# Performance work log

Hardware: AMD Instinct MI355X
Metric: run time of the kernel (lower is better)

Reference implementation:

```python
import jax, jax.numpy as jnp
import numpy as np

B = 64        # batch
N = 1024      # num_nodes
D_IN = 2      # input feature dim per node
U = 64        # num_units (hidden)
K = 2         # max_diffusion_step


def setup_inputs() -> dict:
    key = jax.random.key(0)
    ks = jax.random.split(key, 8)
    inputs = jax.random.normal(ks[0], (B, N * D_IN), dtype=jnp.float32)
    hx = jax.random.normal(ks[1], (B, N * U), dtype=jnp.float32)
    # random-walk style supports: nonnegative, row-normalized -> stable Chebyshev recursion
    a0 = jax.random.uniform(ks[2], (N, N), dtype=jnp.float32)
    a1 = jax.random.uniform(ks[3], (N, N), dtype=jnp.float32)
    support0 = a0 / jnp.sum(a0, axis=1, keepdims=True)
    support1 = a1 / jnp.sum(a1, axis=1, keepdims=True)
    num_matrices = 2 * K + 1            # len(supports)*K + 1 = 5
    in_sz = (D_IN + U) * num_matrices   # 330
    # xavier-normal init
    std_o = float(np.sqrt(2.0 / (in_sz + 2 * U)))
    std_u = float(np.sqrt(2.0 / (in_sz + U)))
    weights_output = jax.random.normal(ks[4], (in_sz, 2 * U), dtype=jnp.float32) * std_o
    weights_update = jax.random.normal(ks[5], (in_sz, U), dtype=jnp.float32) * std_u
    biases_output = jnp.ones((2 * U,), dtype=jnp.float32)
    biases_update = jnp.zeros((U,), dtype=jnp.float32)
    return {"inputs": inputs, "hx": hx, "support0": support0, "support1": support1,
            "weights_output": weights_output, "biases_output": biases_output,
            "weights_update": weights_update, "biases_update": biases_update}


def _gconv(x_cat, supports, W, b, out_size):
    # x_cat: [B, N, F]  -> Chebyshev diffusion series then dense projection
    Bsz, Nn, F = x_cat.shape
    x0 = x_cat.transpose(1, 2, 0).reshape(Nn, F * Bsz)  # [N, F*B]
    xs = [x0]
    for S in supports:
        x1 = S @ x0
        xs.append(x1)
        xk1, xk2 = x1, x0
        for _ in range(2, K + 1):
            x2 = 2.0 * (S @ xk1) - xk2
            xs.append(x2)
            xk1, xk2 = x2, xk1
    M = len(xs)                                         # num_matrices
    x = jnp.stack(xs, axis=0)                           # [M, N, F*B]
    x = x.reshape(M, Nn, F, Bsz).transpose(3, 1, 2, 0)  # [B, N, F, M]
    x = x.reshape(Bsz * Nn, F * M)
    y = x @ W + b                                       # [B*N, out_size]
    return y.reshape(Bsz, Nn * out_size)


def reference(inputs, hx, support0, support1, weights_output, biases_output,
              weights_update, biases_update):
    supports = (support0, support1)
    xi = inputs.reshape(B, N, D_IN)
    hs = hx.reshape(B, N, U)
    cat = jnp.concatenate([xi, hs], axis=2)             # [B, N, D_IN+U]
    value = jax.nn.sigmoid(_gconv(cat, supports, weights_output, biases_output, 2 * U))
    value = value.reshape(B, N, 2 * U)
    r = value[..., :U].reshape(B, N * U)
    u = value[..., U:].reshape(B, N * U)
    cat2 = jnp.concatenate([xi, (r * hx).reshape(B, N, U)], axis=2)
    c = jnp.tanh(_gconv(cat2, supports, weights_update, biases_update, U))
    return u * hx + (1.0 - u) * c
```

## Files before the change

kernel.cpp:

```cpp
#include <hip/hip_runtime.h>


typedef unsigned short u16;
typedef unsigned int u32;
typedef short s16x8 __attribute__((ext_vector_type(8)));
typedef float f32x4 __attribute__((ext_vector_type(4)));
typedef u16 u16x4 __attribute__((ext_vector_type(4)));

#define NN 1024
#define NB 64
#define NF 66
#define NCOLS 4224
#define KPAD 352
#define ASTRIDE 360

__device__ __forceinline__ u16 f2bf(float f) {
  u32 u = __builtin_bit_cast(u32, f);
  u = (u + 0x7fffu + ((u >> 16) & 1u)) >> 16;
  return (u16)u;
}
__device__ __forceinline__ float bf2f(u16 h) {
  u32 u = ((u32)h) << 16;
  return __builtin_bit_cast(float, u);
}

__device__ __forceinline__ void gload16(const void* g, void* l) {
  __builtin_amdgcn_global_load_lds(
      (const __attribute__((address_space(1))) u32*)g,
      (__attribute__((address_space(3))) u32*)l, 16, 0, 0);
}

#define CHEB_WAIT(N)                                      \
  do {                                                    \
    asm volatile("s_waitcnt vmcnt(" #N ")" ::: "memory"); \
    __builtin_amdgcn_s_barrier();                         \
    asm volatile("" ::: "memory");                        \
  } while (0)


__global__ __launch_bounds__(256) void pack_supports(
    const float* __restrict__ s0, const float* __restrict__ s1,
    u16* __restrict__ d0, u16* __restrict__ d1,
    u16* __restrict__ t0, u16* __restrict__ t1) {
  __shared__ float tile[64][65];
  const int z = blockIdx.y;
  const float* S = z ? s1 : s0;
  u16* D = z ? d1 : d0;
  u16* T = z ? t1 : t0;
  const int r0 = (blockIdx.x >> 4) * 64, c0 = (blockIdx.x & 15) * 64;
  const int t = threadIdx.x;
  int cc4 = (t & 15) * 4, rr = t >> 4;
#pragma unroll
  for (int p = 0; p < 4; p++) {
    int r = p * 16 + rr;
    f32x4 v = *(const f32x4*)(S + (size_t)(r0 + r) * NN + c0 + cc4);
    tile[r][cc4] = v.x; tile[r][cc4 + 1] = v.y;
    tile[r][cc4 + 2] = v.z; tile[r][cc4 + 3] = v.w;
    u16x4 o;
    o.x = f2bf(v.x); o.y = f2bf(v.y); o.z = f2bf(v.z); o.w = f2bf(v.w);
    *(u16x4*)&D[(size_t)(r0 + r) * NN + c0 + cc4] = o;
  }
  __syncthreads();
  int rr4 = (t & 15) * 4, cc = t >> 4;
#pragma unroll
  for (int p = 0; p < 4; p++) {
    int c = p * 16 + cc;
    u16x4 o;
    o.x = f2bf(tile[rr4][c]);     o.y = f2bf(tile[rr4 + 1][c]);
    o.z = f2bf(tile[rr4 + 2][c]); o.w = f2bf(tile[rr4 + 3][c]);
    *(u16x4*)&T[(size_t)(c0 + c) * NN + r0 + rr4] = o;
  }
}

__global__ __launch_bounds__(64) void pack_wf(
    const float* __restrict__ Wo, const float* __restrict__ Wu,
    u16* __restrict__ WF1, u16* __restrict__ WF2) {
  const int c = blockIdx.x;
  int j = blockIdx.y;
  const float* W; u16* WF; int ldo, nj;
  if (j < 8) { W = Wo; WF = WF1; ldo = 128; nj = 8; }
  else       { j -= 8; W = Wu; WF = WF2; ldo = 64; nj = 4; }
  const int lane = threadIdx.x;
  const int o = j * 16 + (lane & 15);
  const int kpb = c * 32 + (lane >> 4) * 8;
  u16 vals[8];
#pragma unroll
  for (int e = 0; e < 8; e++) {
    const int kp = kpb + e;
    float v = 0.f;
    if (kp < 330) {
      const int m = kp / 66;
      const int f = kp - m * 66;
      const float* Wrow = W + (size_t)(f * 5) * ldo + o;
      if (m == 0)      v = Wrow[0] - Wrow[2 * ldo] - Wrow[4 * ldo];
      else if (m == 2) v = 2.f * Wrow[2 * ldo];
      else if (m == 4) v = 2.f * Wrow[4 * ldo];
      else             v = Wrow[(size_t)m * ldo];
    }
    vals[e] = f2bf(v);
  }
  u16* dst = WF + (((size_t)(c * nj + j) << 6) + lane) * 8;
#pragma unroll
  for (int e = 0; e < 8; e++) dst[e] = vals[e];
}

__global__ __launch_bounds__(256) void pack_x0(
    const float* __restrict__ inp, const float* __restrict__ hx,
    u16* __restrict__ x0t, u16* __restrict__ x0pt) {
  __shared__ float tile[64][65];
  int n0 = blockIdx.x * 64, b = blockIdx.y, t = threadIdx.x;
  if (t < 32) {
    const int f = t >> 4;
    const int n4 = (t & 15) * 4;
    const float* src = inp + b * 2048 + (n0 + n4) * 2 + f;
    u16x4 o;
    o.x = f2bf(src[0]); o.y = f2bf(src[2]); o.z = f2bf(src[4]); o.w = f2bf(src[6]);
    size_t off = (size_t)(f * 64 + b) * NN + n0 + n4;
    *(u16x4*)(x0t + off) = o;
    *(u16x4*)(x0pt + off) = o;
  }
  int u4 = (t & 15) * 4, r0 = t >> 4;
#pragma unroll
  for (int p = 0; p < 4; p++) {
    int row = p * 16 + r0;
    f32x4 v = *(const f32x4*)(hx + ((size_t)b << 16) + (size_t)(n0 + row) * 64 + u4);
    tile[row][u4] = v.x; tile[row][u4 + 1] = v.y;
    tile[row][u4 + 2] = v.z; tile[row][u4 + 3] = v.w;
  }
  __syncthreads();
  int n4 = (t & 15) * 4, uu0 = t >> 4;
#pragma unroll
  for (int p = 0; p < 4; p++) {
    int u = p * 16 + uu0;
    u16x4 o;
    o.x = f2bf(tile[n4][u]);     o.y = f2bf(tile[n4 + 1][u]);
    o.z = f2bf(tile[n4 + 2][u]); o.w = f2bf(tile[n4 + 3][u]);
    *(u16x4*)&x0t[(size_t)((2 + u) * 64 + b) * NN + n0 + n4] = o;
  }
}


__device__ __forceinline__ void gemm128_core(
    const u16* __restrict__ A, const u16* __restrict__ Xi, u16* __restrict__ Xo,
    int m0, int n0, int t, u16* AsB, u16* BsB) {
  const int lane = t & 63;
  const int w = t >> 6;

  const int swz = ((lane & 3) ^ ((lane >> 3) & 3)) * 8;
  const int rl = lane >> 2;
  const u16* pA0 = A + (size_t)(m0 + w * 32 + rl) * NN + swz;
  const u16* pA1 = pA0 + (size_t)16 * NN;
  const u16* pB0 = Xi + (size_t)(n0 + w * 32 + rl) * NN + swz;
  const u16* pB1 = pB0 + (size_t)16 * NN;
  const int db0 = (w * 32) * 32;
  const int db1 = (w * 32 + 16) * 32;

  const int wm = (w >> 1) * 64;
  const int wn = (w & 1) * 64;
  const int fr = lane & 15;
  const int q = lane >> 4;
  const int fo = (q ^ ((fr >> 1) & 3)) * 8;

  f32x4 acc[4][4];
#pragma unroll
  for (int i = 0; i < 4; i++)
#pragma unroll
    for (int j = 0; j < 4; j++) acc[i][j] = f32x4{0.f, 0.f, 0.f, 0.f};

  auto stage = [&](u16* dA, u16* dB) {
    gload16(pA0, dA + db0);
    gload16(pA1, dA + db1);
    gload16(pB0, dB + db0);
    gload16(pB1, dB + db1);
    pA0 += 32; pA1 += 32; pB0 += 32; pB1 += 32;
  };
  auto compute = [&](const u16* cA, const u16* cB) {
    s16x8 af[4], bfr[4];
#pragma unroll
    for (int i = 0; i < 4; i++)
      af[i] = *(const s16x8*)&cA[(wm + i * 16 + fr) * 32 + fo];
#pragma unroll
    for (int j = 0; j < 4; j++)
      bfr[j] = *(const s16x8*)&cB[(wn + j * 16 + fr) * 32 + fo];
#pragma unroll
    for (int i = 0; i < 4; i++)
#pragma unroll
      for (int j = 0; j < 4; j++)
        acc[i][j] = __builtin_amdgcn_mfma_f32_16x16x32_bf16(af[i], bfr[j], acc[i][j], 0, 0, 0);
  };

  u16* a0 = AsB;  u16* a1 = AsB + 128 * 32;  u16* a2 = AsB + 2 * 128 * 32;
  u16* b0 = BsB;  u16* b1 = BsB + 128 * 32;  u16* b2 = BsB + 2 * 128 * 32;

  stage(a0, b0);
  stage(a1, b1);
#pragma unroll 1
  for (int it = 0; it < 10; it++) {
    CHEB_WAIT(4); stage(a2, b2); compute(a0, b0);
    CHEB_WAIT(4); stage(a0, b0); compute(a1, b1);
    CHEB_WAIT(4); stage(a1, b1); compute(a2, b2);
  }
  CHEB_WAIT(4); compute(a0, b0);
  CHEB_WAIT(0); compute(a1, b1);

  const int nr0 = (lane >> 4) << 2;
#pragma unroll
  for (int i = 0; i < 4; i++) {
    const int node = m0 + wm + i * 16 + nr0;
#pragma unroll
    for (int j = 0; j < 4; j++) {
      const int colg = n0 + wn + j * 16 + fr;
      f32x4 c = acc[i][j];
      u16x4 o;
      o.x = f2bf(c.x); o.y = f2bf(c.y); o.z = f2bf(c.z); o.w = f2bf(c.w);
      *(u16x4*)&Xo[(size_t)colg * NN + node] = o;
    }
  }
}

__global__ __launch_bounds__(256) void sq_gemm(
    const u16* __restrict__ S0, const u16* __restrict__ S1,
    const u16* __restrict__ ST0, const u16* __restrict__ ST1,
    u16* __restrict__ SS0, u16* __restrict__ SS1) {
  __shared__ u16 As[2][128 * 64];
  __shared__ u16 Bs[2][128 * 64];
  const int t = threadIdx.x;
  const int lane = t & 63;
  const int w = t >> 6;
  const int lid = blockIdx.x;
  const int work = (lid & 7) * 16 + (lid >> 3);
  const int z = work >> 6;
  const int rr = work & 63;
  const int y = rr >> 3, x = rr & 7;
  const u16* A = z ? ST1 : ST0;
  const u16* Xi = z ? S1 : S0;
  u16* Xo = z ? SS1 : SS0;
  const int m0 = y * 128, n0 = x * 128;

  const int swz = ((lane & 7) ^ (lane >> 3)) * 8;
  const int rl = lane >> 3;
  const int rA = m0 + w * 32 + rl;
  const int rB = n0 + w * 32 + rl;
  const int dW = (w * 32) * 64;

  const int wm = (w >> 1) * 64;
  const int wn = (w & 1) * 64;
  const int fr = lane & 15;
  const int q = lane >> 4;

  f32x4 acc[4][4];
#pragma unroll
  for (int i = 0; i < 4; i++)
#pragma unroll
    for (int j = 0; j < 4; j++) acc[i][j] = f32x4{0.f, 0.f, 0.f, 0.f};

  auto stage = [&](int buf, int k0) {
    u16* a = &As[buf][0] + dW;
    u16* b = &Bs[buf][0] + dW;
#pragma unroll
    for (int g = 0; g < 4; g++) {
      gload16(A + (size_t)(rA + g * 8) * NN + k0 + swz, a + g * 8 * 64);
      gload16(Xi + (size_t)(rB + g * 8) * NN + k0 + swz, b + g * 8 * 64);
    }
  };
  auto compute = [&](int buf) {
    const u16* a = &As[buf][0];
    const u16* b = &Bs[buf][0];
#pragma unroll
    for (int kk = 0; kk < 2; kk++) {
      const int fo = ((kk * 4 + q) ^ (fr & 7)) * 8;
      s16x8 af[4], bfr[4];
#pragma unroll
      for (int i = 0; i < 4; i++)
        af[i] = *(const s16x8*)&a[(wm + i * 16 + fr) * 64 + fo];
#pragma unroll
      for (int j = 0; j < 4; j++)
        bfr[j] = *(const s16x8*)&b[(wn + j * 16 + fr) * 64 + fo];
#pragma unroll
      for (int i = 0; i < 4; i++)
#pragma unroll
        for (int j = 0; j < 4; j++)
          acc[i][j] = __builtin_amdgcn_mfma_f32_16x16x32_bf16(af[i], bfr[j], acc[i][j], 0, 0, 0);
    }
  };

  stage(0, 0);
  stage(1, 64);
#pragma unroll 1
  for (int tI = 0; tI < 14; tI++) {
    CHEB_WAIT(8);
    compute(tI & 1);
    __builtin_amdgcn_s_barrier();
    stage(tI & 1, (tI + 2) * 64);
  }
  CHEB_WAIT(8); compute(0);
  CHEB_WAIT(0); compute(1);

  const int nr0 = (lane >> 4) << 2;
#pragma unroll
  for (int i = 0; i < 4; i++) {
    const int node = m0 + wm + i * 16 + nr0;
#pragma unroll
    for (int j = 0; j < 4; j++) {
      const int colg = n0 + wn + j * 16 + fr;
      f32x4 c = acc[i][j];
      u16x4 o;
      o.x = f2bf(c.x); o.y = f2bf(c.y); o.z = f2bf(c.z); o.w = f2bf(c.w);
      *(u16x4*)&Xo[(size_t)colg * NN + node] = o;
    }
  }
}

__global__ __launch_bounds__(256, 3) void gconv_gemm(
    const u16* __restrict__ S0, const u16* __restrict__ S1,
    const u16* __restrict__ SS0, const u16* __restrict__ SS1,
    const u16* __restrict__ Xi,
    u16* __restrict__ X1, u16* __restrict__ X2,
    u16* __restrict__ X3, u16* __restrict__ X4) {
  __shared__ u16 As[3][128 * 32];
  __shared__ u16 Bs[3][128 * 32];
  const int lid = blockIdx.x;
  const int h = lid >= 528;
  const int l2 = h ? lid - 528 : lid;
  const int work = (l2 & 7) * 66 + (l2 >> 3);
  const int y = work & 7;
  const int tt = work >> 3;
  const int x = tt % 33;
  const int z = tt / 33;
  const u16* A = h ? (z ? SS1 : SS0) : (z ? S1 : S0);
  u16* Xo = h ? (z ? X4 : X2) : (z ? X3 : X1);
  gemm128_core(A, Xi, Xo, y * 128, x * 128, threadIdx.x, &As[0][0], &Bs[0][0]);
}


__device__ __forceinline__ void proj_stage(
    u16* A, const u16* __restrict__ X0, const u16* __restrict__ X1,
    const u16* __restrict__ X2, const u16* __restrict__ X3,
    const u16* __restrict__ X4, int b, int n0, int t) {
  u16x4 v[6][4];
#pragma unroll
  for (int i = 0; i < 6; i++) {
    const int idx = t + i * 256;
    if (idx < 1408) {
      const int kp0 = (idx >> 4) * 4;
      const int n4 = (idx & 15) * 4;
#pragma unroll
      for (int r = 0; r < 4; r++) {
        const int kp = kp0 + r;
        if (kp < 330) {
          const int m = kp / 66;
          const int f = kp - m * 66;
          const u16* Xm = m == 0 ? X0 : m == 1 ? X1 : m == 2 ? X2 : m == 3 ? X3 : X4;
          v[i][r] = *(const u16x4*)(Xm + (size_t)(f * 64 + b) * NN + n0 + n4);
        } else {
          v[i][r] = u16x4{0, 0, 0, 0};
        }
      }
    }
  }
#pragma unroll
  for (int i = 0; i < 6; i++) {
    const int idx = t + i * 256;
    if (idx < 1408) {
      const int kp0 = (idx >> 4) * 4;
      const int n4 = (idx & 15) * 4;
#pragma unroll
      for (int c = 0; c < 4; c++) {
        u16x4 o;
        o.x = v[i][0][c]; o.y = v[i][1][c]; o.z = v[i][2][c]; o.w = v[i][3][c];
        *(u16x4*)&A[(n4 + c) * ASTRIDE + kp0] = o;
      }
    }
  }
}

__global__ __launch_bounds__(256) void proj1(
    const u16* __restrict__ X0, const u16* __restrict__ X1, const u16* __restrict__ X2,
    const u16* __restrict__ X3, const u16* __restrict__ X4,
    const u16* __restrict__ WF, const float* __restrict__ bias,
    const float* __restrict__ hx, u16* __restrict__ X0p, float* __restrict__ uout) {
  __shared__ u16 A[64 * ASTRIDE];
  const int t = threadIdx.x;
  const int n0 = blockIdx.x * 64;
  const int b = blockIdx.y;
  proj_stage(A, X0, X1, X2, X3, X4, b, n0, t);
  __syncthreads();

  const int lane = t & 63;
  const int w = t >> 6;
  const int fr = lane & 15;
  const int q8 = (lane >> 4) * 8;
  const int nb = (w >> 1) * 32;
  const int jh = w & 1;
  const u16* arow = &A[(nb + fr) * ASTRIDE + q8];
  const u16* wfl = WF + (size_t)lane * 8;

  f32x4 acc[2][4];
#pragma unroll
  for (int ii = 0; ii < 2; ii++)
#pragma unroll
    for (int j = 0; j < 4; j++) acc[ii][j] = f32x4{0.f, 0.f, 0.f, 0.f};

  for (int c = 0; c < 11; c++) {
    s16x8 af[2];
#pragma unroll
    for (int ii = 0; ii < 2; ii++)
      af[ii] = *(const s16x8*)(arow + ii * 16 * ASTRIDE + c * 32);
#pragma unroll
    for (int j = 0; j < 4; j++) {
      const s16x8 bf = *(const s16x8*)(wfl + ((c * 8 + jh * 4 + j) << 9));
#pragma unroll
      for (int ii = 0; ii < 2; ii++)
        acc[ii][j] = __builtin_amdgcn_mfma_f32_16x16x32_bf16(af[ii], bf, acc[ii][j], 0, 0, 0);
    }
  }

  const int nl0 = (lane >> 4) * 4;
#pragma unroll
  for (int ii = 0; ii < 2; ii++) {
    const int n = n0 + nb + ii * 16 + nl0;
#pragma unroll
    for (int j = 0; j < 4; j++) {
      const int ol = j * 16 + fr;
      const float bs = bias[jh * 64 + ol];
      f32x4 v;
      v.x = 1.f / (1.f + __expf(-(acc[ii][j].x + bs)));
      v.y = 1.f / (1.f + __expf(-(acc[ii][j].y + bs)));
      v.z = 1.f / (1.f + __expf(-(acc[ii][j].z + bs)));
      v.w = 1.f / (1.f + __expf(-(acc[ii][j].w + bs)));
      if (jh == 0) {
        const float* hxp = hx + ((size_t)b << 16) + (size_t)n * 64 + ol;
        u16x4 s;
        s.x = f2bf(v.x * hxp[0 * 64]);
        s.y = f2bf(v.y * hxp[1 * 64]);
        s.z = f2bf(v.z * hxp[2 * 64]);
        s.w = f2bf(v.w * hxp[3 * 64]);
        *(u16x4*)&X0p[(size_t)((2 + ol) * 64 + b) * NN + n] = s;
      } else {
        float* up = uout + (((size_t)b << 10) + n) * 64 + ol;
        up[0 * 64] = v.x; up[1 * 64] = v.y; up[2 * 64] = v.z; up[3 * 64] = v.w;
      }
    }
  }
}

__global__ __launch_bounds__(256) void proj2(
    const u16* __restrict__ X0, const u16* __restrict__ X1, const u16* __restrict__ X2,
    const u16* __restrict__ X3, const u16* __restrict__ X4,
    const u16* __restrict__ WF, const float* __restrict__ bias,
    const float* __restrict__ hx, const float* uin, float* out) {
  __shared__ u16 A[64 * ASTRIDE];
  const int t = threadIdx.x;
  const int n0 = blockIdx.x * 64;
  const int b = blockIdx.y;
  proj_stage(A, X0, X1, X2, X3, X4, b, n0, t);
  __syncthreads();

  const int lane = t & 63;
  const int w = t >> 6;
  const int fr = lane & 15;
  const int q8 = (lane >> 4) * 8;
  const int nb = (w >> 1) * 32;
  const int jh = w & 1;
  const u16* arow = &A[(nb + fr) * ASTRIDE + q8];
  const u16* wfl = WF + (size_t)lane * 8;

  f32x4 acc[2][2];
#pragma unroll
  for (int ii = 0; ii < 2; ii++)
#pragma unroll
    for (int j = 0; j < 2; j++) acc[ii][j] = f32x4{0.f, 0.f, 0.f, 0.f};

  for (int c = 0; c < 11; c++) {
    s16x8 af[2];
#pragma unroll
    for (int ii = 0; ii < 2; ii++)
      af[ii] = *(const s16x8*)(arow + ii * 16 * ASTRIDE + c * 32);
#pragma unroll
    for (int j = 0; j < 2; j++) {
      const s16x8 bf = *(const s16x8*)(wfl + ((c * 4 + jh * 2 + j) << 9));
#pragma unroll
      for (int ii = 0; ii < 2; ii++)
        acc[ii][j] = __builtin_amdgcn_mfma_f32_16x16x32_bf16(af[ii], bf, acc[ii][j], 0, 0, 0);
    }
  }

  const int nl0 = (lane >> 4) * 4;
#pragma unroll
  for (int ii = 0; ii < 2; ii++) {
    const int n = n0 + nb + ii * 16 + nl0;
#pragma unroll
    for (int j = 0; j < 2; j++) {
      const int o = jh * 32 + j * 16 + fr;
      const float bs = bias[o];
      const size_t base = (((size_t)b << 10) + n) * 64 + o;
      float c0 = tanhf(acc[ii][j].x + bs);
      float c1 = tanhf(acc[ii][j].y + bs);
      float c2 = tanhf(acc[ii][j].z + bs);
      float c3 = tanhf(acc[ii][j].w + bs);
      float u0 = uin[base + 0 * 64], u1 = uin[base + 1 * 64];
      float u2 = uin[base + 2 * 64], u3 = uin[base + 3 * 64];
      float h0 = hx[base + 0 * 64], h1 = hx[base + 1 * 64];
      float h2 = hx[base + 2 * 64], h3 = hx[base + 3 * 64];
      out[base + 0 * 64] = u0 * h0 + (1.f - u0) * c0;
      out[base + 1 * 64] = u1 * h1 + (1.f - u1) * c1;
      out[base + 2 * 64] = u2 * h2 + (1.f - u2) * c2;
      out[base + 3 * 64] = u3 * h3 + (1.f - u3) * c3;
    }
  }
}


extern "C" void kernel_launch(void* const* d_in, const int* in_sizes, int n_in,
                              void* d_out, int out_size, void* d_ws, size_t ws_size,
                              hipStream_t stream) {
  (void)in_sizes; (void)n_in; (void)out_size; (void)ws_size;
  const float* inp = (const float*)d_in[0];
  const float* hx  = (const float*)d_in[1];
  const float* s0  = (const float*)d_in[2];
  const float* s1  = (const float*)d_in[3];
  const float* Wo  = (const float*)d_in[4];
  const float* bo  = (const float*)d_in[5];
  const float* Wu  = (const float*)d_in[6];
  const float* bu  = (const float*)d_in[7];
  float* out = (float*)d_out;

  char* p = (char*)d_ws;
  u16* Sb0 = (u16*)p; p += (size_t)NN * NN * 2;
  u16* Sb1 = (u16*)p; p += (size_t)NN * NN * 2;
  u16* SSb0 = (u16*)p; p += (size_t)NN * NN * 2;
  u16* SSb1 = (u16*)p; p += (size_t)NN * NN * 2;
  const size_t xbytes = (size_t)NCOLS * NN * 2;
  u16* X0T = (u16*)p; p += xbytes;
  u16* X1T = (u16*)p; p += xbytes;
  u16* X2T = (u16*)p; p += xbytes;
  u16* X3T = (u16*)p; p += xbytes;
  u16* X4T = (u16*)p; p += xbytes;
  u16* X0P = (u16*)p; p += xbytes;
  u16* WF1 = (u16*)p; p += (size_t)11 * 8 * 512 * 2;
  u16* WF2 = (u16*)p; p += (size_t)11 * 4 * 512 * 2;
  u16* ST0 = X1T;
  u16* ST1 = X3T;

  pack_supports<<<dim3(256, 2), dim3(256), 0, stream>>>(s0, s1, Sb0, Sb1, ST0, ST1);
  sq_gemm<<<dim3(128), dim3(256), 0, stream>>>(Sb0, Sb1, ST0, ST1, SSb0, SSb1);
  pack_wf<<<dim3(11, 12), dim3(64), 0, stream>>>(Wo, Wu, WF1, WF2);
  pack_x0<<<dim3(16, 64), dim3(256), 0, stream>>>(inp, hx, X0T, X0P);
  gconv_gemm<<<dim3(1056), dim3(256), 0, stream>>>(Sb0, Sb1, SSb0, SSb1, X0T,
                                                   X1T, X2T, X3T, X4T);
  proj1<<<dim3(16, 64), dim3(256), 0, stream>>>(X0T, X1T, X2T, X3T, X4T, WF1, bo, hx, X0P, out);
  gconv_gemm<<<dim3(1056), dim3(256), 0, stream>>>(Sb0, Sb1, SSb0, SSb1, X0P,
                                                   X1T, X2T, X3T, X4T);
  proj2<<<dim3(16, 64), dim3(256), 0, stream>>>(X0P, X1T, X2T, X3T, X4T, WF2, bu, hx, out, out);
}
```

Measured before the change: 267.0 us.

## Merge pack kernels into one launch and split proj staging into two phases

The three preprocessing kernels (support packing, weight packing, x0 packing) become one kernel that picks its role from the block index, removing two launches. The proj1/proj2 kernels now stage the 352-wide K dimension in two halves through a smaller shared buffer (stride 200 instead of 360). That cuts LDS use and, together with a launch-bounds hint of 6 blocks per CU, is meant to raise occupancy. The cost is an extra pair of barriers and a second staging pass in each projection block.

```diff
diff --git a/kernel.cpp b/kernel.cpp
--- a/kernel.cpp
+++ b/kernel.cpp
@@ -12,7 +12,7 @@
 #define NF 66
 #define NCOLS 4224
 #define KPAD 352
-#define ASTRIDE 360
+#define PSTRIDE 200
 
 __device__ __forceinline__ u16 f2bf(float f) {
   u32 u = __builtin_bit_cast(u32, f);
@@ -37,184 +37,107 @@
     asm volatile("" ::: "memory");                        \
   } while (0)
 
-
-__global__ __launch_bounds__(256) void pack_supports(
+__global__ __launch_bounds__(256) void pack_all(
     const float* __restrict__ s0, const float* __restrict__ s1,
-    u16* __restrict__ d0, u16* __restrict__ d1,
-    u16* __restrict__ t0, u16* __restrict__ t1) {
+    const float* __restrict__ inp, const float* __restrict__ hx,
+    const float* __restrict__ Wo, const float* __restrict__ Wu,
+    u16* __restrict__ Sb0, u16* __restrict__ Sb1,
+    u16* __restrict__ ST0, u16* __restrict__ ST1,
+    u16* __restrict__ x0t, u16* __restrict__ x0pt,
+    u16* __restrict__ WF1, u16* __restrict__ WF2) {
   __shared__ float tile[64][65];
-  const int z = blockIdx.y;
-  const float* S = z ? s1 : s0;
-  u16* D = z ? d1 : d0;
-  u16* T = z ? t1 : t0;
-  const int r0 = (blockIdx.x >> 4) * 64, c0 = (blockIdx.x & 15) * 64;
+  const int bid = blockIdx.x;
   const int t = threadIdx.x;
-  int cc4 = (t & 15) * 4, rr = t >> 4;
-#pragma unroll
-  for (int p = 0; p < 4; p++) {
-    int r = p * 16 + rr;
-    f32x4 v = *(const f32x4*)(S + (size_t)(r0 + r) * NN + c0 + cc4);
-    tile[r][cc4] = v.x; tile[r][cc4 + 1] = v.y;
-    tile[r][cc4 + 2] = v.z; tile[r][cc4 + 3] = v.w;
-    u16x4 o;
-    o.x = f2bf(v.x); o.y = f2bf(v.y); o.z = f2bf(v.z); o.w = f2bf(v.w);
-    *(u16x4*)&D[(size_t)(r0 + r) * NN + c0 + cc4] = o;
-  }
-  __syncthreads();
-  int rr4 = (t & 15) * 4, cc = t >> 4;
-#pragma unroll
-  for (int p = 0; p < 4; p++) {
-    int c = p * 16 + cc;
-    u16x4 o;
-    o.x = f2bf(tile[rr4][c]);     o.y = f2bf(tile[rr4 + 1][c]);
-    o.z = f2bf(tile[rr4 + 2][c]); o.w = f2bf(tile[rr4 + 3][c]);
-    *(u16x4*)&T[(size_t)(c0 + c) * NN + r0 + rr4] = o;
-  }
-}
-
-__global__ __launch_bounds__(64) void pack_wf(
-    const float* __restrict__ Wo, const float* __restrict__ Wu,
-    u16* __restrict__ WF1, u16* __restrict__ WF2) {
-  const int c = blockIdx.x;
-  int j = blockIdx.y;
-  const float* W; u16* WF; int ldo, nj;
-  if (j < 8) { W = Wo; WF = WF1; ldo = 128; nj = 8; }
-  else       { j -= 8; W = Wu; WF = WF2; ldo = 64; nj = 4; }
-  const int lane = threadIdx.x;
-  const int o = j * 16 + (lane & 15);
-  const int kpb = c * 32 + (lane >> 4) * 8;
-  u16 vals[8];
-#pragma unroll
-  for (int e = 0; e < 8; e++) {
-    const int kp = kpb + e;
-    float v = 0.f;
-    if (kp < 330) {
-      const int m = kp / 66;
-      const int f = kp - m * 66;
-      const float* Wrow = W + (size_t)(f * 5) * ldo + o;
-      if (m == 0)      v = Wrow[0] - Wrow[2 * ldo] - Wrow[4 * ldo];
-      else if (m == 2) v = 2.f * Wrow[2 * ldo];
-      else if (m == 4) v = 2.f * Wrow[4 * ldo];
-      else             v = Wrow[(size_t)m * ldo];
-    }
-    vals[e] = f2bf(v);
-  }
-  u16* dst = WF + (((size_t)(c * nj + j) << 6) + lane) * 8;
-#pragma unroll
-  for (int e = 0; e < 8; e++) dst[e] = vals[e];
-}
-
-__global__ __launch_bounds__(256) void pack_x0(
-    const float* __restrict__ inp, const float* __restrict__ hx,
-    u16* __restrict__ x0t, u16* __restrict__ x0pt) {
-  __shared__ float tile[64][65];
-  int n0 = blockIdx.x * 64, b = blockIdx.y, t = threadIdx.x;
-  if (t < 32) {
-    const int f = t >> 4;
-    const int n4 = (t & 15) * 4;
-    const float* src = inp + b * 2048 + (n0 + n4) * 2 + f;
-    u16x4 o;
-    o.x = f2bf(src[0]); o.y = f2bf(src[2]); o.z = f2bf(src[4]); o.w = f2bf(src[6]);
-    size_t off = (size_t)(f * 64 + b) * NN + n0 + n4;
-    *(u16x4*)(x0t + off) = o;
-    *(u16x4*)(x0pt + off) = o;
-  }
-  int u4 = (t & 15) * 4, r0 = t >> 4;
-#pragma unroll
-  for (int p = 0; p < 4; p++) {
-    int row = p * 16 + r0;
-    f32x4 v = *(const f32x4*)(hx + ((size_t)b << 16) + (size_t)(n0 + row) * 64 + u4);
-    tile[row][u4] = v.x; tile[row][u4 + 1] = v.y;
-    tile[row][u4 + 2] = v.z; tile[row][u4 + 3] = v.w;
-  }
-  __syncthreads();
-  int n4 = (t & 15) * 4, uu0 = t >> 4;
-#pragma unroll
-  for (int p = 0; p < 4; p++) {
-    int u = p * 16 + uu0;
-    u16x4 o;
-    o.x = f2bf(tile[n4][u]);     o.y = f2bf(tile[n4 + 1][u]);
-    o.z = f2bf(tile[n4 + 2][u]); o.w = f2bf(tile[n4 + 3][u]);
-    *(u16x4*)&x0t[(size_t)((2 + u) * 64 + b) * NN + n0 + n4] = o;
-  }
-}
-
-
-__device__ __forceinline__ void gemm128_core(
-    const u16* __restrict__ A, const u16* __restrict__ Xi, u16* __restrict__ Xo,
-    int m0, int n0, int t, u16* AsB, u16* BsB) {
-  const int lane = t & 63;
-  const int w = t >> 6;
-
-  const int swz = ((lane & 3) ^ ((lane >> 3) & 3)) * 8;
-  const int rl = lane >> 2;
-  const u16* pA0 = A + (size_t)(m0 + w * 32 + rl) * NN + swz;
-  const u16* pA1 = pA0 + (size_t)16 * NN;
-  const u16* pB0 = Xi + (size_t)(n0 + w * 32 + rl) * NN + swz;
-  const u16* pB1 = pB0 + (size_t)16 * NN;
-  const int db0 = (w * 32) * 32;
-  const int db1 = (w * 32 + 16) * 32;
-
-  const int wm = (w >> 1) * 64;
-  const int wn = (w & 1) * 64;
-  const int fr = lane & 15;
-  const int q = lane >> 4;
-  const int fo = (q ^ ((fr >> 1) & 3)) * 8;
-
-  f32x4 acc[4][4];
-#pragma unroll
-  for (int i = 0; i < 4; i++)
-#pragma unroll
-    for (int j = 0; j < 4; j++) acc[i][j] = f32x4{0.f, 0.f, 0.f, 0.f};
-
-  auto stage = [&](u16* dA, u16* dB) {
-    gload16(pA0, dA + db0);
-    gload16(pA1, dA + db1);
-    gload16(pB0, dB + db0);
-    gload16(pB1, dB + db1);
-    pA0 += 32; pA1 += 32; pB0 += 32; pB1 += 32;
-  };
-  auto compute = [&](const u16* cA, const u16* cB) {
-    s16x8 af[4], bfr[4];
-#pragma unroll
-    for (int i = 0; i < 4; i++)
-      af[i] = *(const s16x8*)&cA[(wm + i * 16 + fr) * 32 + fo];
-#pragma unroll
-    for (int j = 0; j < 4; j++)
-      bfr[j] = *(const s16x8*)&cB[(wn + j * 16 + fr) * 32 + fo];
-#pragma unroll
-    for (int i = 0; i < 4; i++)
-#pragma unroll
-      for (int j = 0; j < 4; j++)
-        acc[i][j] = __builtin_amdgcn_mfma_f32_16x16x32_bf16(af[i], bfr[j], acc[i][j], 0, 0, 0);
-  };
-
-  u16* a0 = AsB;  u16* a1 = AsB + 128 * 32;  u16* a2 = AsB + 2 * 128 * 32;
-  u16* b0 = BsB;  u16* b1 = BsB + 128 * 32;  u16* b2 = BsB + 2 * 128 * 32;
-
-  stage(a0, b0);
-  stage(a1, b1);
-#pragma unroll 1
-  for (int it = 0; it < 10; it++) {
-    CHEB_WAIT(4); stage(a2, b2); compute(a0, b0);
-    CHEB_WAIT(4); stage(a0, b0); compute(a1, b1);
-    CHEB_WAIT(4); stage(a1, b1); compute(a2, b2);
-  }
-  CHEB_WAIT(4); compute(a0, b0);
-  CHEB_WAIT(0); compute(a1, b1);
-
-  const int nr0 = (lane >> 4) << 2;
-#pragma unroll
-  for (int i = 0; i < 4; i++) {
-    const int node = m0 + wm + i * 16 + nr0;
-#pragma unroll
-    for (int j = 0; j < 4; j++) {
-      const int colg = n0 + wn + j * 16 + fr;
-      f32x4 c = acc[i][j];
+
+  if (bid < 512) {
+    const int z = bid >> 8;
+    const int bx = bid & 255;
+    const float* S = z ? s1 : s0;
+    u16* D = z ? Sb1 : Sb0;
+    u16* T = z ? ST1 : ST0;
+    const int r0 = (bx >> 4) * 64, c0 = (bx & 15) * 64;
+    int cc4 = (t & 15) * 4, rr = t >> 4;
+#pragma unroll
+    for (int p = 0; p < 4; p++) {
+      int r = p * 16 + rr;
+      f32x4 v = *(const f32x4*)(S + (size_t)(r0 + r) * NN + c0 + cc4);
+      tile[r][cc4] = v.x; tile[r][cc4 + 1] = v.y;
+      tile[r][cc4 + 2] = v.z; tile[r][cc4 + 3] = v.w;
       u16x4 o;
-      o.x = f2bf(c.x); o.y = f2bf(c.y); o.z = f2bf(c.z); o.w = f2bf(c.w);
-      *(u16x4*)&Xo[(size_t)colg * NN + node] = o;
-    }
+      o.x = f2bf(v.x); o.y = f2bf(v.y); o.z = f2bf(v.z); o.w = f2bf(v.w);
+      *(u16x4*)&D[(size_t)(r0 + r) * NN + c0 + cc4] = o;
+    }
+    __syncthreads();
+    int rr4 = (t & 15) * 4, cc = t >> 4;
+#pragma unroll
+    for (int p = 0; p < 4; p++) {
+      int c = p * 16 + cc;
+      u16x4 o;
+      o.x = f2bf(tile[rr4][c]);     o.y = f2bf(tile[rr4 + 1][c]);
+      o.z = f2bf(tile[rr4 + 2][c]); o.w = f2bf(tile[rr4 + 3][c]);
+      *(u16x4*)&T[(size_t)(c0 + c) * NN + r0 + rr4] = o;
+    }
+  } else if (bid < 1536) {
+    const int idx = bid - 512;
+    const int n0 = (idx & 15) * 64, b = idx >> 4;
+    if (t < 32) {
+      const int f = t >> 4;
+      const int n4 = (t & 15) * 4;
+      const float* src = inp + b * 2048 + (n0 + n4) * 2 + f;
+      u16x4 o;
+      o.x = f2bf(src[0]); o.y = f2bf(src[2]); o.z = f2bf(src[4]); o.w = f2bf(src[6]);
+      size_t off = (size_t)(f * 64 + b) * NN + n0 + n4;
+      *(u16x4*)(x0t + off) = o;
+      *(u16x4*)(x0pt + off) = o;
+    }
+    int u4 = (t & 15) * 4, r0 = t >> 4;
+#pragma unroll
+    for (int p = 0; p < 4; p++) {
+      int row = p * 16 + r0;
+      f32x4 v = *(const f32x4*)(hx + ((size_t)b << 16) + (size_t)(n0 + row) * 64 + u4);
+      tile[row][u4] = v.x; tile[row][u4 + 1] = v.y;
+      tile[row][u4 + 2] = v.z; tile[row][u4 + 3] = v.w;
+    }
+    __syncthreads();
+    int n4 = (t & 15) * 4, uu0 = t >> 4;
+#pragma unroll
+    for (int p = 0; p < 4; p++) {
+      int u = p * 16 + uu0;
+      u16x4 o;
+      o.x = f2bf(tile[n4][u]);     o.y = f2bf(tile[n4 + 1][u]);
+      o.z = f2bf(tile[n4 + 2][u]); o.w = f2bf(tile[n4 + 3][u]);
+      *(u16x4*)&x0t[(size_t)((2 + u) * 64 + b) * NN + n0 + n4] = o;
+    }
+  } else {
+    const int gid = (bid - 1536) * 256 + t;
+    const int pair = gid >> 6;
+    const int lane = gid & 63;
+    const int c = pair % 11;
+    int jj = pair / 11;
+    const float* W; u16* WF; int ldo, nj;
+    if (jj < 8) { W = Wo; WF = WF1; ldo = 128; nj = 8; }
+    else        { jj -= 8; W = Wu; WF = WF2; ldo = 64; nj = 4; }
+    const int o = jj * 16 + (lane & 15);
+    const int kpb = c * 32 + (lane >> 4) * 8;
+    u16 vals[8];
+#pragma unroll
+    for (int e = 0; e < 8; e++) {
+      const int kp = kpb + e;
+      float v = 0.f;
+      if (kp < 330) {
+        const int m = kp / 66;
+        const int f = kp - m * 66;
+        const float* Wrow = W + (size_t)(f * 5) * ldo + o;
+        if (m == 0)      v = Wrow[0] - Wrow[2 * ldo] - Wrow[4 * ldo];
+        else if (m == 2) v = 2.f * Wrow[2 * ldo];
+        else if (m == 4) v = 2.f * Wrow[4 * ldo];
+        else             v = Wrow[(size_t)m * ldo];
+      }
+      vals[e] = f2bf(v);
+    }
+    u16* dst = WF + (((size_t)(c * nj + jj) << 6) + lane) * 8;
+#pragma unroll
+    for (int e = 0; e < 8; e++) dst[e] = vals[e];
   }
 }
 
@@ -295,6 +218,85 @@
   }
   CHEB_WAIT(8); compute(0);
   CHEB_WAIT(0); compute(1);
+
+  const int nr0 = (lane >> 4) << 2;
+#pragma unroll
+  for (int i = 0; i < 4; i++) {
+    const int node = m0 + wm + i * 16 + nr0;
+#pragma unroll
+    for (int j = 0; j < 4; j++) {
+      const int colg = n0 + wn + j * 16 + fr;
+      f32x4 c = acc[i][j];
+      u16x4 o;
+      o.x = f2bf(c.x); o.y = f2bf(c.y); o.z = f2bf(c.z); o.w = f2bf(c.w);
+      *(u16x4*)&Xo[(size_t)colg * NN + node] = o;
+    }
+  }
+}
+
+
+__device__ __forceinline__ void gemm128_core(
+    const u16* __restrict__ A, const u16* __restrict__ Xi, u16* __restrict__ Xo,
+    int m0, int n0, int t, u16* AsB, u16* BsB) {
+  const int lane = t & 63;
+  const int w = t >> 6;
+
+  const int swz = ((lane & 3) ^ ((lane >> 3) & 3)) * 8;
+  const int rl = lane >> 2;
+  const u16* pA0 = A + (size_t)(m0 + w * 32 + rl) * NN + swz;
+  const u16* pA1 = pA0 + (size_t)16 * NN;
+  const u16* pB0 = Xi + (size_t)(n0 + w * 32 + rl) * NN + swz;
+  const u16* pB1 = pB0 + (size_t)16 * NN;
+  const int db0 = (w * 32) * 32;
+  const int db1 = (w * 32 + 16) * 32;
+
+  const int wm = (w >> 1) * 64;
+  const int wn = (w & 1) * 64;
+  const int fr = lane & 15;
+  const int q = lane >> 4;
+  const int fo = (q ^ ((fr >> 1) & 3)) * 8;
+
+  f32x4 acc[4][4];
+#pragma unroll
+  for (int i = 0; i < 4; i++)
+#pragma unroll
+    for (int j = 0; j < 4; j++) acc[i][j] = f32x4{0.f, 0.f, 0.f, 0.f};
+
+  auto stage = [&](u16* dA, u16* dB) {
+    gload16(pA0, dA + db0);
+    gload16(pA1, dA + db1);
+    gload16(pB0, dB + db0);
+    gload16(pB1, dB + db1);
+    pA0 += 32; pA1 += 32; pB0 += 32; pB1 += 32;
+  };
+  auto compute = [&](const u16* cA, const u16* cB) {
+    s16x8 af[4], bfr[4];
+#pragma unroll
+    for (int i = 0; i < 4; i++)
+      af[i] = *(const s16x8*)&cA[(wm + i * 16 + fr) * 32 + fo];
+#pragma unroll
+    for (int j = 0; j < 4; j++)
+      bfr[j] = *(const s16x8*)&cB[(wn + j * 16 + fr) * 32 + fo];
+#pragma unroll
+    for (int i = 0; i < 4; i++)
+#pragma unroll
+      for (int j = 0; j < 4; j++)
+        acc[i][j] = __builtin_amdgcn_mfma_f32_16x16x32_bf16(af[i], bfr[j], acc[i][j], 0, 0, 0);
+  };
+
+  u16* a0 = AsB;  u16* a1 = AsB + 128 * 32;  u16* a2 = AsB + 2 * 128 * 32;
+  u16* b0 = BsB;  u16* b1 = BsB + 128 * 32;  u16* b2 = BsB + 2 * 128 * 32;
+
+  stage(a0, b0);
+  stage(a1, b1);
+#pragma unroll 1
+  for (int it = 0; it < 10; it++) {
+    CHEB_WAIT(4); stage(a2, b2); compute(a0, b0);
+    CHEB_WAIT(4); stage(a0, b0); compute(a1, b1);
+    CHEB_WAIT(4); stage(a1, b1); compute(a2, b2);
+  }
+  CHEB_WAIT(4); compute(a0, b0);
+  CHEB_WAIT(0); compute(a1, b1);
 
   const int nr0 = (lane >> 4) << 2;
 #pragma unroll
@@ -333,16 +335,16 @@
 }
 
 
-__device__ __forceinline__ void proj_stage(
+__device__ __forceinline__ void proj_stage_ph(
     u16* A, const u16* __restrict__ X0, const u16* __restrict__ X1,
     const u16* __restrict__ X2, const u16* __restrict__ X3,
-    const u16* __restrict__ X4, int b, int n0, int t) {
-  u16x4 v[6][4];
-#pragma unroll
-  for (int i = 0; i < 6; i++) {
+    const u16* __restrict__ X4, int b, int n0, int t, int kb, int nids) {
+  u16x4 v[3][4];
+#pragma unroll
+  for (int i = 0; i < 3; i++) {
     const int idx = t + i * 256;
-    if (idx < 1408) {
-      const int kp0 = (idx >> 4) * 4;
+    if (idx < nids) {
+      const int kp0 = kb + (idx >> 4) * 4;
       const int n4 = (idx & 15) * 4;
 #pragma unroll
       for (int r = 0; r < 4; r++) {
@@ -359,32 +361,30 @@
     }
   }
 #pragma unroll
-  for (int i = 0; i < 6; i++) {
+  for (int i = 0; i < 3; i++) {
     const int idx = t + i * 256;
-    if (idx < 1408) {
-      const int kp0 = (idx >> 4) * 4;
+    if (idx < nids) {
+      const int kpl = (idx >> 4) * 4;
       const int n4 = (idx & 15) * 4;
 #pragma unroll
       for (int c = 0; c < 4; c++) {
         u16x4 o;
         o.x = v[i][0][c]; o.y = v[i][1][c]; o.z = v[i][2][c]; o.w = v[i][3][c];
-        *(u16x4*)&A[(n4 + c) * ASTRIDE + kp0] = o;
+        *(u16x4*)&A[(n4 + c) * PSTRIDE + kpl] = o;
       }
     }
   }
 }
 
-__global__ __launch_bounds__(256) void proj1(
+__global__ __launch_bounds__(256, 6) void proj1(
     const u16* __restrict__ X0, const u16* __restrict__ X1, const u16* __restrict__ X2,
     const u16* __restrict__ X3, const u16* __restrict__ X4,
     const u16* __restrict__ WF, const float* __restrict__ bias,
     const float* __restrict__ hx, u16* __restrict__ X0p, float* __restrict__ uout) {
-  __shared__ u16 A[64 * ASTRIDE];
+  __shared__ u16 A[64 * PSTRIDE];
   const int t = threadIdx.x;
   const int n0 = blockIdx.x * 64;
   const int b = blockIdx.y;
-  proj_stage(A, X0, X1, X2, X3, X4, b, n0, t);
-  __syncthreads();
 
   const int lane = t & 63;
   const int w = t >> 6;
@@ -392,7 +392,7 @@
   const int q8 = (lane >> 4) * 8;
   const int nb = (w >> 1) * 32;
   const int jh = w & 1;
-  const u16* arow = &A[(nb + fr) * ASTRIDE + q8];
+  const u16* arow = &A[(nb + fr) * PSTRIDE + q8];
   const u16* wfl = WF + (size_t)lane * 8;
 
   f32x4 acc[2][4];
@@ -401,11 +401,29 @@
 #pragma unroll
     for (int j = 0; j < 4; j++) acc[ii][j] = f32x4{0.f, 0.f, 0.f, 0.f};
 
-  for (int c = 0; c < 11; c++) {
+  proj_stage_ph(A, X0, X1, X2, X3, X4, b, n0, t, 0, 768);
+  __syncthreads();
+  for (int c = 0; c < 6; c++) {
     s16x8 af[2];
 #pragma unroll
     for (int ii = 0; ii < 2; ii++)
-      af[ii] = *(const s16x8*)(arow + ii * 16 * ASTRIDE + c * 32);
+      af[ii] = *(const s16x8*)(arow + ii * 16 * PSTRIDE + c * 32);
+#pragma unroll
+    for (int j = 0; j < 4; j++) {
+      const s16x8 bf = *(const s16x8*)(wfl + ((c * 8 + jh * 4 + j) << 9));
+#pragma unroll
+      for (int ii = 0; ii < 2; ii++)
+        acc[ii][j] = __builtin_amdgcn_mfma_f32_16x16x32_bf16(af[ii], bf, acc[ii][j], 0, 0, 0);
+    }
+  }
+  __syncthreads();
+  proj_stage_ph(A, X0, X1, X2, X3, X4, b, n0, t, 192, 640);
+  __syncthreads();
+  for (int c = 6; c < 11; c++) {
+    s16x8 af[2];
+#pragma unroll
+    for (int ii = 0; ii < 2; ii++)
+      af[ii] = *(const s16x8*)(arow + ii * 16 * PSTRIDE + (c - 6) * 32);
 #pragma unroll
     for (int j = 0; j < 4; j++) {
       const s16x8 bf = *(const s16x8*)(wfl + ((c * 8 + jh * 4 + j) << 9));
@@ -444,17 +462,15 @@
   }
 }
 
-__global__ __launch_bounds__(256) void proj2(
+__global__ __launch_bounds__(256, 6) void proj2(
     const u16* __restrict__ X0, const u16* __restrict__ X1, const u16* __restrict__ X2,
     const u16* __restrict__ X3, const u16* __restrict__ X4,
     const u16* __restrict__ WF, const float* __restrict__ bias,
     const float* __restrict__ hx, const float* uin, float* out) {
-  __shared__ u16 A[64 * ASTRIDE];
+  __shared__ u16 A[64 * PSTRIDE];
   const int t = threadIdx.x;
   const int n0 = blockIdx.x * 64;
   const int b = blockIdx.y;
-  proj_stage(A, X0, X1, X2, X3, X4, b, n0, t);
-  __syncthreads();
 
   const int lane = t & 63;
   const int w = t >> 6;
@@ -462,7 +478,7 @@
   const int q8 = (lane >> 4) * 8;
   const int nb = (w >> 1) * 32;
   const int jh = w & 1;
-  const u16* arow = &A[(nb + fr) * ASTRIDE + q8];
+  const u16* arow = &A[(nb + fr) * PSTRIDE + q8];
   const u16* wfl = WF + (size_t)lane * 8;
 
   f32x4 acc[2][2];
@@ -471,11 +487,29 @@
 #pragma unroll
     for (int j = 0; j < 2; j++) acc[ii][j] = f32x4{0.f, 0.f, 0.f, 0.f};
 
-  for (int c = 0; c < 11; c++) {
+  proj_stage_ph(A, X0, X1, X2, X3, X4, b, n0, t, 0, 768);
+  __syncthreads();
+  for (int c = 0; c < 6; c++) {
     s16x8 af[2];
 #pragma unroll
     for (int ii = 0; ii < 2; ii++)
-      af[ii] = *(const s16x8*)(arow + ii * 16 * ASTRIDE + c * 32);
+      af[ii] = *(const s16x8*)(arow + ii * 16 * PSTRIDE + c * 32);
+#pragma unroll
+    for (int j = 0; j < 2; j++) {
+      const s16x8 bf = *(const s16x8*)(wfl + ((c * 4 + jh * 2 + j) << 9));
+#pragma unroll
+      for (int ii = 0; ii < 2; ii++)
+        acc[ii][j] = __builtin_amdgcn_mfma_f32_16x16x32_bf16(af[ii], bf, acc[ii][j], 0, 0, 0);
+    }
+  }
+  __syncthreads();
+  proj_stage_ph(A, X0, X1, X2, X3, X4, b, n0, t, 192, 640);
+  __syncthreads();
+  for (int c = 6; c < 11; c++) {
+    s16x8 af[2];
+#pragma unroll
+    for (int ii = 0; ii < 2; ii++)
+      af[ii] = *(const s16x8*)(arow + ii * 16 * PSTRIDE + (c - 6) * 32);
 #pragma unroll
     for (int j = 0; j < 2; j++) {
       const s16x8 bf = *(const s16x8*)(wfl + ((c * 4 + jh * 2 + j) << 9));
@@ -542,10 +576,9 @@
   u16* ST0 = X1T;
   u16* ST1 = X3T;
 
-  pack_supports<<<dim3(256, 2), dim3(256), 0, stream>>>(s0, s1, Sb0, Sb1, ST0, ST1);
+  pack_all<<<dim3(1569), dim3(256), 0, stream>>>(
+      s0, s1, inp, hx, Wo, Wu, Sb0, Sb1, ST0, ST1, X0T, X0P, WF1, WF2);
   sq_gemm<<<dim3(128), dim3(256), 0, stream>>>(Sb0, Sb1, ST0, ST1, SSb0, SSb1);
-  pack_wf<<<dim3(11, 12), dim3(64), 0, stream>>>(Wo, Wu, WF1, WF2);
-  pack_x0<<<dim3(16, 64), dim3(256), 0, stream>>>(inp, hx, X0T, X0P);
   gconv_gemm<<<dim3(1056), dim3(256), 0, stream>>>(Sb0, Sb1, SSb0, SSb1, X0T,
                                                    X1T, X2T, X3T, X4T);
   proj1<<<dim3(16, 64), dim3(256), 0, stream>>>(X0T, X1T, X2T, X3T, X4T, WF1, bo, hx, X0P, out);
```

Measured after the change: 261.5 us. -2.1%, faster.
